# Kernel tuning notes

Hardware: AMD Instinct MI355X
Metric: run time of the kernel (lower is better)

## Reference

```python
import jax, jax.numpy as jnp
import numpy as np

EPS = 1e-12  # torch F.normalize eps

def _l2norm(x):
    n = jnp.linalg.norm(x, axis=-1, keepdims=True)
    return x / jnp.maximum(n, EPS)

def _encode(h, mask, W, b):
    # h: [B,S,H], mask: [B,S] int
    h = h * mask[..., None].astype(h.dtype)      # zero padded tokens
    pooled = h[:, 0]                             # pooling_type='cls'
    col = h[:, 1:] @ W + b                       # colbert_linear on tokens 1:
    return _l2norm(pooled), _l2norm(col)         # normalize=True


def setup_inputs() -> dict:
    key = jax.random.key(0)
    k1, k2, k3, k4, k5, k6 = jax.random.split(key, 6)
    Q, Sq, C, Sc, H, D = 64, 32, 256, 256, 768, 128
    return {
        "q_hidden": jax.random.normal(k1, (Q, Sq, H), jnp.float32),
        "c_hidden": jax.random.normal(k2, (C, Sc, H), jnp.float32),
        "W": jax.random.normal(k3, (H, D), jnp.float32) / np.sqrt(H).astype(np.float32),
        "b": jax.random.normal(k4, (D,), jnp.float32) * 0.01,
        "q_mask": jax.random.randint(k5, (Q, Sq), 0, 2, jnp.int32),
        "c_mask": jax.random.randint(k6, (C, Sc), 0, 2, jnp.int32),
    }


def reference(q_hidden, c_hidden, W, b, q_mask, c_mask):
    q_pooled, q_col = _encode(q_hidden, q_mask, W, b)   # q_col: [Q, Sq-1, D]
    c_pooled, c_col = _encode(c_hidden, c_mask, W, b)   # c_col: [C, Sc-1, D]
    # MaxSim late interaction (get_batch_colbert_sim)
    token_sim = jnp.einsum('qin,cjn->qicj', q_col, c_col)  # [Q, Sq-1, C, Sc-1]
    sim = token_sim.max(axis=-1)                           # max over doc tokens j
    denom = q_mask[:, 1:].sum(-1, keepdims=True).astype(sim.dtype)
    sim = sim.sum(axis=1) / denom                          # [Q, C]
    return sim, q_pooled, c_pooled
```

## Files before the change

### kernel.cpp

```cpp
#include <hip/hip_runtime.h>
#include <hip/hip_bf16.h>

#define QN 64
#define SQ 32
#define CN 256
#define SC 256
#define HD 768
#define DD 128

typedef __attribute__((ext_vector_type(8))) short short8;
typedef __attribute__((ext_vector_type(4))) float f32x4;

static __device__ __forceinline__ unsigned short f2bf(float x) {
  unsigned u = __float_as_uint(x);
  unsigned r = 0x7FFFu + ((u >> 16) & 1u);
  return (unsigned short)((u + r) >> 16);
}
static __device__ __forceinline__ unsigned pack2(float a, float b) {
  return (unsigned)f2bf(a) | ((unsigned)f2bf(b) << 16);
}

__global__ __launch_bounds__(256) void wcvt_kernel(const float* __restrict__ W,
                                                   unsigned short* __restrict__ Wt) {
  int d = blockIdx.x;
  for (int k = threadIdx.x; k < HD; k += 256)
    Wt[d * HD + k] = f2bf(W[(size_t)k * DD + d]);
}

__global__ __launch_bounds__(256) void pooled_kernel(
    const float* __restrict__ qh, const int* __restrict__ qm,
    const float* __restrict__ ch, const int* __restrict__ cm,
    float* __restrict__ outq, float* __restrict__ outc,
    unsigned short* __restrict__ qcolP) {
  int bid = blockIdx.x;
  const float* src;
  float* dst;
  float m;
  if (bid < QN) {
    src = qh + (size_t)bid * SQ * HD;
    m = (float)qm[bid * SQ];
    dst = outq + (size_t)bid * HD;
  } else {
    int b = bid - QN;
    src = ch + (size_t)b * SC * HD;
    m = (float)cm[b * SC];
    dst = outc + (size_t)b * HD;
  }
  int tid = threadIdx.x;
  float ss = 0.f;
  for (int k = tid; k < HD; k += 256) {
    float v = src[k] * m;
    ss += v * v;
  }
  __shared__ float red[4];
  int lane = tid & 63, wv = tid >> 6;
  for (int off = 32; off; off >>= 1) ss += __shfl_xor(ss, off);
  if (lane == 0) red[wv] = ss;
  __syncthreads();
  float tot = red[0] + red[1] + red[2] + red[3];
  float inv = 1.f / fmaxf(sqrtf(tot), 1e-12f);
  for (int k = tid; k < HD; k += 256) dst[k] = src[k] * m * inv;
  if (bid < QN && tid < 64)
    ((unsigned*)(qcolP + ((size_t)bid * 32 + 31) * DD))[tid] = 0u;
}

union ProjLDS {
  struct { unsigned short a[64 * 64]; unsigned short b[128 * 64]; } s;
  float c[64 * 132];
};

__global__ __launch_bounds__(256) void proj_kernel(
    const float* __restrict__ hidden, const int* __restrict__ mask,
    const unsigned short* __restrict__ Wt, const float* __restrict__ bias,
    unsigned short* __restrict__ out, int S, int flag) {
  __shared__ ProjLDS u;
  int tid = threadIdx.x, lane = tid & 63, w = tid >> 6;
  int lm = lane & 15, lq = lane >> 4;
  int T = S - 1;
  int wm = w & 1, wn = w >> 1;

  int ar = tid >> 2, aseg = tid & 3;
  int ag = blockIdx.x * 64 + ar;
  int ab = ag / T, at = ag - ab * T;
  const float* hrow = hidden + ((size_t)ab * S + at + 1) * HD;
  float am = (float)mask[ab * S + at + 1];
  int bd = tid >> 1, bh = tid & 1;
  const unsigned short* wrow = Wt + (size_t)bd * HD + bh * 32;

  f32x4 acc[2][4];
#pragma unroll
  for (int i = 0; i < 2; ++i)
#pragma unroll
    for (int j = 0; j < 4; ++j) acc[i][j] = (f32x4){0.f, 0.f, 0.f, 0.f};

  for (int k0 = 0; k0 < HD; k0 += 64) {
    __syncthreads();
    {
      const float4* hp = (const float4*)(hrow + k0 + aseg * 16);
      float4 v0 = hp[0], v1 = hp[1], v2 = hp[2], v3 = hp[3];
      unsigned p[8];
      p[0] = pack2(v0.x * am, v0.y * am); p[1] = pack2(v0.z * am, v0.w * am);
      p[2] = pack2(v1.x * am, v1.y * am); p[3] = pack2(v1.z * am, v1.w * am);
      p[4] = pack2(v2.x * am, v2.y * am); p[5] = pack2(v2.z * am, v2.w * am);
      p[6] = pack2(v3.x * am, v3.y * am); p[7] = pack2(v3.z * am, v3.w * am);
      int kc0 = aseg * 2;
      int pk0 = kc0 ^ (ar & 7), pk1 = (kc0 + 1) ^ (ar & 7);
      *(uint4*)&u.s.a[(ar * 8 + pk0) * 8] = *(uint4*)&p[0];
      *(uint4*)&u.s.a[(ar * 8 + pk1) * 8] = *(uint4*)&p[4];
    }
    {
      const uint4* wp = (const uint4*)(wrow + k0);
#pragma unroll
      for (int j = 0; j < 4; ++j) {
        int kc = bh * 4 + j;
        int pk = kc ^ (bd & 7);
        *(uint4*)&u.s.b[(bd * 8 + pk) * 8] = wp[j];
      }
    }
    __syncthreads();
#pragma unroll
    for (int kf = 0; kf < 2; ++kf) {
      short8 a2[2], b4[4];
#pragma unroll
      for (int mt = 0; mt < 2; ++mt) {
        int row = (wm * 2 + mt) * 16 + lm;
        int kc = kf * 4 + lq;
        a2[mt] = *(const short8*)&u.s.a[(row * 8 + (kc ^ (row & 7))) * 8];
      }
#pragma unroll
      for (int nt = 0; nt < 4; ++nt) {
        int row = (wn * 4 + nt) * 16 + lm;
        int kc = kf * 4 + lq;
        b4[nt] = *(const short8*)&u.s.b[(row * 8 + (kc ^ (row & 7))) * 8];
      }
#pragma unroll
      for (int mt = 0; mt < 2; ++mt)
#pragma unroll
        for (int nt = 0; nt < 4; ++nt)
          acc[mt][nt] = __builtin_amdgcn_mfma_f32_16x16x32_bf16(a2[mt], b4[nt], acc[mt][nt], 0, 0, 0);
    }
  }

  __syncthreads();
#pragma unroll
  for (int mt = 0; mt < 2; ++mt)
#pragma unroll
    for (int nt = 0; nt < 4; ++nt)
#pragma unroll
      for (int r = 0; r < 4; ++r) {
        int row = (wm * 2 + mt) * 16 + lq * 4 + r;
        int col = (wn * 4 + nt) * 16 + lm;
        u.c[row * 132 + col] = acc[mt][nt][r];
      }
  __syncthreads();

  int r2 = tid >> 2, seg2 = tid & 3;
  float v[32];
  float ss = 0.f;
#pragma unroll
  for (int j = 0; j < 8; ++j) {
    float4 cv = *(const float4*)&u.c[r2 * 132 + seg2 * 32 + j * 4];
    float4 bv = *(const float4*)&bias[seg2 * 32 + j * 4];
    v[4 * j + 0] = cv.x + bv.x; v[4 * j + 1] = cv.y + bv.y;
    v[4 * j + 2] = cv.z + bv.z; v[4 * j + 3] = cv.w + bv.w;
#pragma unroll
    for (int e = 0; e < 4; ++e) ss += v[4 * j + e] * v[4 * j + e];
  }
  ss += __shfl_xor(ss, 1);
  ss += __shfl_xor(ss, 2);
  float inv = 1.f / fmaxf(sqrtf(ss), 1e-12f);

  unsigned pk[16];
#pragma unroll
  for (int j = 0; j < 16; ++j) pk[j] = pack2(v[2 * j] * inv, v[2 * j + 1] * inv);

  int g = blockIdx.x * 64 + r2;
  int b = g / T, tt = g - b * T;
  unsigned short* dst;
  if (!flag)
    dst = out + ((size_t)b * 32 + tt) * DD + seg2 * 32;
  else
    dst = out + ((size_t)b * 256 + tt) * DD + seg2 * 32;
  uint4* d4 = (uint4*)dst;
  d4[0] = *(uint4*)&pk[0];  d4[1] = *(uint4*)&pk[4];
  d4[2] = *(uint4*)&pk[8];  d4[3] = *(uint4*)&pk[12];
  if (flag && tt == 254) {
    uint4* d5 = (uint4*)(dst + DD);
    d5[0] = *(uint4*)&pk[0];  d5[1] = *(uint4*)&pk[4];
    d5[2] = *(uint4*)&pk[8];  d5[3] = *(uint4*)&pk[12];
  }
}

__global__ __launch_bounds__(256, 2) void sim_kernel(
    const unsigned short* __restrict__ qcolP,
    const unsigned short* __restrict__ ccol,
    const int* __restrict__ qmask,
    float* __restrict__ sim) {
  __shared__ unsigned short cbuf[256 * 128];
  int tid = threadIdx.x, lane = tid & 63, w = tid >> 6;
  int lm = lane & 15, lq = lane >> 4;
  int q0 = blockIdx.y * 8 + w * 2;
  int c0 = blockIdx.x * 4;

  short8 af[2][2][4];
#pragma unroll
  for (int q2 = 0; q2 < 2; ++q2)
#pragma unroll
    for (int it = 0; it < 2; ++it)
#pragma unroll
      for (int kf = 0; kf < 4; ++kf)
        af[q2][it][kf] = *(const short8*)(qcolP +
            (((size_t)(q0 + q2) * 32 + it * 16 + lm) * DD + kf * 32 + lq * 8));

  float dinv[2];
#pragma unroll
  for (int q2 = 0; q2 < 2; ++q2) {
    float v = (lane >= 1 && lane < 32) ? (float)qmask[(q0 + q2) * SQ + lane] : 0.f;
    for (int off = 1; off < 64; off <<= 1) v += __shfl_xor(v, off);
    dinv[q2] = 1.f / v;
  }

  for (int cc = 0; cc < 4; ++cc) {
    int c = c0 + cc;
    __syncthreads();
    const uint4* src = (const uint4*)(ccol + (size_t)c * SC * DD);
#pragma unroll
    for (int half = 0; half < 2; ++half) {
      uint4 tmp[8];
#pragma unroll
      for (int it = 0; it < 8; ++it) tmp[it] = src[(half * 8 + it) * 256 + tid];
#pragma unroll
      for (int it = 0; it < 8; ++it) {
        int idx = (half * 8 + it) * 256 + tid;
        int row = idx >> 4, kc = idx & 15;
        int pkc = (kc & 8) | ((kc & 7) ^ (row & 7));
        *(uint4*)&cbuf[(row * 16 + pkc) * 8] = tmp[it];
      }
    }
    __syncthreads();

    float cmx[2][2][4];
#pragma unroll
    for (int q2 = 0; q2 < 2; ++q2)
#pragma unroll
      for (int it = 0; it < 2; ++it)
#pragma unroll
        for (int r = 0; r < 4; ++r) cmx[q2][it][r] = -__builtin_inff();

    for (int jt = 0; jt < 16; ++jt) {
      short8 bf[4];
#pragma unroll
      for (int kf = 0; kf < 4; ++kf) {
        int row = jt * 16 + lm;
        int kc = kf * 4 + lq;
        int pkc = (kc & 8) | ((kc & 7) ^ (row & 7));
        bf[kf] = *(const short8*)&cbuf[(row * 16 + pkc) * 8];
      }
#pragma unroll
      for (int q2 = 0; q2 < 2; ++q2)
#pragma unroll
        for (int it = 0; it < 2; ++it) {
          f32x4 acc = (f32x4){0.f, 0.f, 0.f, 0.f};
#pragma unroll
          for (int kf = 0; kf < 4; ++kf)
            acc = __builtin_amdgcn_mfma_f32_16x16x32_bf16(af[q2][it][kf], bf[kf], acc, 0, 0, 0);
#pragma unroll
          for (int r = 0; r < 4; ++r) cmx[q2][it][r] = fmaxf(cmx[q2][it][r], acc[r]);
        }
    }

#pragma unroll
    for (int q2 = 0; q2 < 2; ++q2) {
#pragma unroll
      for (int off = 1; off < 16; off <<= 1)
#pragma unroll
        for (int it = 0; it < 2; ++it)
#pragma unroll
          for (int r = 0; r < 4; ++r)
            cmx[q2][it][r] = fmaxf(cmx[q2][it][r], __shfl_xor(cmx[q2][it][r], off));
      float s = cmx[q2][0][0] + cmx[q2][0][1] + cmx[q2][0][2] + cmx[q2][0][3]
              + cmx[q2][1][0] + cmx[q2][1][1] + cmx[q2][1][2]
              + ((lq == 3) ? 0.f : cmx[q2][1][3]);
      s += __shfl_xor(s, 16);
      s += __shfl_xor(s, 32);
      if (lane == 0) sim[(q0 + q2) * CN + c] = s * dinv[q2];
    }
  }
}

extern "C" void kernel_launch(void* const* d_in, const int* in_sizes, int n_in,
                              void* d_out, int out_size, void* d_ws, size_t ws_size,
                              hipStream_t stream) {
  const float* q_hidden = (const float*)d_in[0];
  const float* c_hidden = (const float*)d_in[1];
  const float* W = (const float*)d_in[2];
  const float* bias = (const float*)d_in[3];
  const int* q_mask = (const int*)d_in[4];
  const int* c_mask = (const int*)d_in[5];

  float* out = (float*)d_out;
  float* sim = out;
  float* q_pooled = out + QN * CN;
  float* c_pooled = q_pooled + QN * HD;

  unsigned short* Wt    = (unsigned short*)d_ws;
  unsigned short* qcolP = (unsigned short*)((char*)d_ws + (256 << 10));
  unsigned short* ccol  = (unsigned short*)((char*)d_ws + (1 << 20));

  wcvt_kernel<<<DD, 256, 0, stream>>>(W, Wt);
  pooled_kernel<<<QN + CN, 256, 0, stream>>>(q_hidden, q_mask, c_hidden, c_mask,
                                             q_pooled, c_pooled, qcolP);
  proj_kernel<<<31, 256, 0, stream>>>(q_hidden, q_mask, Wt, bias, qcolP, SQ, 0);
  proj_kernel<<<1020, 256, 0, stream>>>(c_hidden, c_mask, Wt, bias, ccol, SC, 1);
  sim_kernel<<<dim3(64, 8), 256, 0, stream>>>(qcolP, ccol, q_mask, sim);
}
```

Measured before the change: 381.6 us.

## Merge prep and projection launches, prefetch proj tiles, restructure sim kernel

```diff
diff --git a/kernel.cpp b/kernel.cpp
--- a/kernel.cpp
+++ b/kernel.cpp
@@ -20,39 +20,41 @@
   return (unsigned)f2bf(a) | ((unsigned)f2bf(b) << 16);
 }
 
-__global__ __launch_bounds__(256) void wcvt_kernel(const float* __restrict__ W,
-                                                   unsigned short* __restrict__ Wt) {
-  int d = blockIdx.x;
-  for (int k = threadIdx.x; k < HD; k += 256)
-    Wt[d * HD + k] = f2bf(W[(size_t)k * DD + d]);
-}
-
-__global__ __launch_bounds__(256) void pooled_kernel(
+__global__ __launch_bounds__(256) void prep_kernel(
+    const float* __restrict__ W,
     const float* __restrict__ qh, const int* __restrict__ qm,
     const float* __restrict__ ch, const int* __restrict__ cm,
+    unsigned short* __restrict__ Wt,
     float* __restrict__ outq, float* __restrict__ outc,
     unsigned short* __restrict__ qcolP) {
-  int bid = blockIdx.x;
+  __shared__ float red[4];
+  int bid = blockIdx.x, tid = threadIdx.x;
+
+  if (bid < DD) {
+    for (int k = tid; k < HD; k += 256)
+      Wt[bid * HD + k] = f2bf(W[(size_t)k * DD + bid]);
+    return;
+  }
+
+  int row = bid - DD;
   const float* src;
   float* dst;
   float m;
-  if (bid < QN) {
-    src = qh + (size_t)bid * SQ * HD;
-    m = (float)qm[bid * SQ];
-    dst = outq + (size_t)bid * HD;
+  if (row < QN) {
+    src = qh + (size_t)row * SQ * HD;
+    m = (float)qm[row * SQ];
+    dst = outq + (size_t)row * HD;
   } else {
-    int b = bid - QN;
+    int b = row - QN;
     src = ch + (size_t)b * SC * HD;
     m = (float)cm[b * SC];
     dst = outc + (size_t)b * HD;
   }
-  int tid = threadIdx.x;
   float ss = 0.f;
   for (int k = tid; k < HD; k += 256) {
     float v = src[k] * m;
     ss += v * v;
   }
-  __shared__ float red[4];
   int lane = tid & 63, wv = tid >> 6;
   for (int off = 32; off; off >>= 1) ss += __shfl_xor(ss, off);
   if (lane == 0) red[wv] = ss;
@@ -60,8 +62,8 @@
   float tot = red[0] + red[1] + red[2] + red[3];
   float inv = 1.f / fmaxf(sqrtf(tot), 1e-12f);
   for (int k = tid; k < HD; k += 256) dst[k] = src[k] * m * inv;
-  if (bid < QN && tid < 64)
-    ((unsigned*)(qcolP + ((size_t)bid * 32 + 31) * DD))[tid] = 0u;
+  if (row < QN && tid < 64)
+    ((unsigned*)(qcolP + ((size_t)row * 32 + 31) * DD))[tid] = 0u;
 }
 
 union ProjLDS {
@@ -70,19 +72,29 @@
 };
 
 __global__ __launch_bounds__(256) void proj_kernel(
-    const float* __restrict__ hidden, const int* __restrict__ mask,
+    const float* __restrict__ q_hidden, const float* __restrict__ c_hidden,
+    const int* __restrict__ q_mask, const int* __restrict__ c_mask,
     const unsigned short* __restrict__ Wt, const float* __restrict__ bias,
-    unsigned short* __restrict__ out, int S, int flag) {
+    unsigned short* __restrict__ qcol, unsigned short* __restrict__ ccol) {
   __shared__ ProjLDS u;
+  int bx = blockIdx.x;
+  int isQ = (bx >= 1020) ? 1 : 0;
+  int base = isQ ? (bx - 1020) : bx;
+  const float* hidden = isQ ? q_hidden : c_hidden;
+  const int* mask = isQ ? q_mask : c_mask;
+  int S = isQ ? SQ : SC;
+  int T = S - 1;
+  int OUTS = isQ ? 32 : 256;
+  unsigned short* out = isQ ? qcol : ccol;
+
   int tid = threadIdx.x, lane = tid & 63, w = tid >> 6;
   int lm = lane & 15, lq = lane >> 4;
-  int T = S - 1;
   int wm = w & 1, wn = w >> 1;
 
   int ar = tid >> 2, aseg = tid & 3;
-  int ag = blockIdx.x * 64 + ar;
+  int ag = base * 64 + ar;
   int ab = ag / T, at = ag - ab * T;
-  const float* hrow = hidden + ((size_t)ab * S + at + 1) * HD;
+  const float* hrow = hidden + ((size_t)ab * S + at + 1) * HD + aseg * 16;
   float am = (float)mask[ab * S + at + 1];
   int bd = tid >> 1, bh = tid & 1;
   const unsigned short* wrow = Wt + (size_t)bd * HD + bh * 32;
@@ -93,31 +105,41 @@
 #pragma unroll
     for (int j = 0; j < 4; ++j) acc[i][j] = (f32x4){0.f, 0.f, 0.f, 0.f};
 
+  float4 va[4];
+  uint4 vb[4];
+#pragma unroll
+  for (int j = 0; j < 4; ++j) va[j] = ((const float4*)hrow)[j];
+#pragma unroll
+  for (int j = 0; j < 4; ++j) vb[j] = ((const uint4*)wrow)[j];
+
   for (int k0 = 0; k0 < HD; k0 += 64) {
     __syncthreads();
     {
-      const float4* hp = (const float4*)(hrow + k0 + aseg * 16);
-      float4 v0 = hp[0], v1 = hp[1], v2 = hp[2], v3 = hp[3];
       unsigned p[8];
-      p[0] = pack2(v0.x * am, v0.y * am); p[1] = pack2(v0.z * am, v0.w * am);
-      p[2] = pack2(v1.x * am, v1.y * am); p[3] = pack2(v1.z * am, v1.w * am);
-      p[4] = pack2(v2.x * am, v2.y * am); p[5] = pack2(v2.z * am, v2.w * am);
-      p[6] = pack2(v3.x * am, v3.y * am); p[7] = pack2(v3.z * am, v3.w * am);
+      p[0] = pack2(va[0].x * am, va[0].y * am); p[1] = pack2(va[0].z * am, va[0].w * am);
+      p[2] = pack2(va[1].x * am, va[1].y * am); p[3] = pack2(va[1].z * am, va[1].w * am);
+      p[4] = pack2(va[2].x * am, va[2].y * am); p[5] = pack2(va[2].z * am, va[2].w * am);
+      p[6] = pack2(va[3].x * am, va[3].y * am); p[7] = pack2(va[3].z * am, va[3].w * am);
       int kc0 = aseg * 2;
       int pk0 = kc0 ^ (ar & 7), pk1 = (kc0 + 1) ^ (ar & 7);
       *(uint4*)&u.s.a[(ar * 8 + pk0) * 8] = *(uint4*)&p[0];
       *(uint4*)&u.s.a[(ar * 8 + pk1) * 8] = *(uint4*)&p[4];
-    }
-    {
-      const uint4* wp = (const uint4*)(wrow + k0);
 #pragma unroll
       for (int j = 0; j < 4; ++j) {
         int kc = bh * 4 + j;
         int pk = kc ^ (bd & 7);
-        *(uint4*)&u.s.b[(bd * 8 + pk) * 8] = wp[j];
+        *(uint4*)&u.s.b[(bd * 8 + pk) * 8] = vb[j];
       }
     }
     __syncthreads();
+    if (k0 + 64 < HD) {
+      const float4* hp = (const float4*)(hrow + k0 + 64);
+      const uint4* wp = (const uint4*)(wrow + k0 + 64);
+#pragma unroll
+      for (int j = 0; j < 4; ++j) va[j] = hp[j];
+#pragma unroll
+      for (int j = 0; j < 4; ++j) vb[j] = wp[j];
+    }
 #pragma unroll
     for (int kf = 0; kf < 2; ++kf) {
       short8 a2[2], b4[4];
@@ -174,24 +196,20 @@
 #pragma unroll
   for (int j = 0; j < 16; ++j) pk[j] = pack2(v[2 * j] * inv, v[2 * j + 1] * inv);
 
-  int g = blockIdx.x * 64 + r2;
+  int g = base * 64 + r2;
   int b = g / T, tt = g - b * T;
-  unsigned short* dst;
-  if (!flag)
-    dst = out + ((size_t)b * 32 + tt) * DD + seg2 * 32;
-  else
-    dst = out + ((size_t)b * 256 + tt) * DD + seg2 * 32;
+  unsigned short* dst = out + ((size_t)b * OUTS + tt) * DD + seg2 * 32;
   uint4* d4 = (uint4*)dst;
   d4[0] = *(uint4*)&pk[0];  d4[1] = *(uint4*)&pk[4];
   d4[2] = *(uint4*)&pk[8];  d4[3] = *(uint4*)&pk[12];
-  if (flag && tt == 254) {
+  if (!isQ && tt == 254) {
     uint4* d5 = (uint4*)(dst + DD);
     d5[0] = *(uint4*)&pk[0];  d5[1] = *(uint4*)&pk[4];
     d5[2] = *(uint4*)&pk[8];  d5[3] = *(uint4*)&pk[12];
   }
 }
 
-__global__ __launch_bounds__(256, 2) void sim_kernel(
+__global__ __launch_bounds__(128, 1) void sim_kernel(
     const unsigned short* __restrict__ qcolP,
     const unsigned short* __restrict__ ccol,
     const int* __restrict__ qmask,
@@ -199,23 +217,23 @@
   __shared__ unsigned short cbuf[256 * 128];
   int tid = threadIdx.x, lane = tid & 63, w = tid >> 6;
   int lm = lane & 15, lq = lane >> 4;
-  int q0 = blockIdx.y * 8 + w * 2;
+  int qb = blockIdx.y * 8 + w * 4;
   int c0 = blockIdx.x * 4;
 
-  short8 af[2][2][4];
-#pragma unroll
-  for (int q2 = 0; q2 < 2; ++q2)
+  short8 af[4][2][4];
+#pragma unroll
+  for (int q2 = 0; q2 < 4; ++q2)
 #pragma unroll
     for (int it = 0; it < 2; ++it)
 #pragma unroll
       for (int kf = 0; kf < 4; ++kf)
         af[q2][it][kf] = *(const short8*)(qcolP +
-            (((size_t)(q0 + q2) * 32 + it * 16 + lm) * DD + kf * 32 + lq * 8));
-
-  float dinv[2];
-#pragma unroll
-  for (int q2 = 0; q2 < 2; ++q2) {
-    float v = (lane >= 1 && lane < 32) ? (float)qmask[(q0 + q2) * SQ + lane] : 0.f;
+            (((size_t)(qb + q2) * 32 + it * 16 + lm) * DD + kf * 32 + lq * 8));
+
+  float dinv[4];
+#pragma unroll
+  for (int q2 = 0; q2 < 4; ++q2) {
+    float v = (lane >= 1 && lane < 32) ? (float)qmask[(qb + q2) * SQ + lane] : 0.f;
     for (int off = 1; off < 64; off <<= 1) v += __shfl_xor(v, off);
     dinv[q2] = 1.f / v;
   }
@@ -225,13 +243,13 @@
     __syncthreads();
     const uint4* src = (const uint4*)(ccol + (size_t)c * SC * DD);
 #pragma unroll
-    for (int half = 0; half < 2; ++half) {
+    for (int g4 = 0; g4 < 4; ++g4) {
       uint4 tmp[8];
 #pragma unroll
-      for (int it = 0; it < 8; ++it) tmp[it] = src[(half * 8 + it) * 256 + tid];
+      for (int it = 0; it < 8; ++it) tmp[it] = src[(g4 * 8 + it) * 128 + tid];
 #pragma unroll
       for (int it = 0; it < 8; ++it) {
-        int idx = (half * 8 + it) * 256 + tid;
+        int idx = (g4 * 8 + it) * 128 + tid;
         int row = idx >> 4, kc = idx & 15;
         int pkc = (kc & 8) | ((kc & 7) ^ (row & 7));
         *(uint4*)&cbuf[(row * 16 + pkc) * 8] = tmp[it];
@@ -239,51 +257,41 @@
     }
     __syncthreads();
 
-    float cmx[2][2][4];
-#pragma unroll
-    for (int q2 = 0; q2 < 2; ++q2)
-#pragma unroll
-      for (int it = 0; it < 2; ++it)
-#pragma unroll
-        for (int r = 0; r < 4; ++r) cmx[q2][it][r] = -__builtin_inff();
+    float rmax[4][2];
+#pragma unroll
+    for (int q2 = 0; q2 < 4; ++q2) { rmax[q2][0] = -__builtin_inff(); rmax[q2][1] = -__builtin_inff(); }
 
     for (int jt = 0; jt < 16; ++jt) {
-      short8 bf[4];
+      short8 cf[4];
 #pragma unroll
       for (int kf = 0; kf < 4; ++kf) {
         int row = jt * 16 + lm;
         int kc = kf * 4 + lq;
         int pkc = (kc & 8) | ((kc & 7) ^ (row & 7));
-        bf[kf] = *(const short8*)&cbuf[(row * 16 + pkc) * 8];
-      }
-#pragma unroll
-      for (int q2 = 0; q2 < 2; ++q2)
+        cf[kf] = *(const short8*)&cbuf[(row * 16 + pkc) * 8];
+      }
+#pragma unroll
+      for (int q2 = 0; q2 < 4; ++q2)
 #pragma unroll
         for (int it = 0; it < 2; ++it) {
           f32x4 acc = (f32x4){0.f, 0.f, 0.f, 0.f};
 #pragma unroll
           for (int kf = 0; kf < 4; ++kf)
-            acc = __builtin_amdgcn_mfma_f32_16x16x32_bf16(af[q2][it][kf], bf[kf], acc, 0, 0, 0);
-#pragma unroll
-          for (int r = 0; r < 4; ++r) cmx[q2][it][r] = fmaxf(cmx[q2][it][r], acc[r]);
+            acc = __builtin_amdgcn_mfma_f32_16x16x32_bf16(cf[kf], af[q2][it][kf], acc, 0, 0, 0);
+          float loc = fmaxf(fmaxf(acc[0], acc[1]), fmaxf(acc[2], acc[3]));
+          rmax[q2][it] = fmaxf(rmax[q2][it], loc);
         }
     }
 
 #pragma unroll
-    for (int q2 = 0; q2 < 2; ++q2) {
-#pragma unroll
-      for (int off = 1; off < 16; off <<= 1)
-#pragma unroll
-        for (int it = 0; it < 2; ++it)
-#pragma unroll
-          for (int r = 0; r < 4; ++r)
-            cmx[q2][it][r] = fmaxf(cmx[q2][it][r], __shfl_xor(cmx[q2][it][r], off));
-      float s = cmx[q2][0][0] + cmx[q2][0][1] + cmx[q2][0][2] + cmx[q2][0][3]
-              + cmx[q2][1][0] + cmx[q2][1][1] + cmx[q2][1][2]
-              + ((lq == 3) ? 0.f : cmx[q2][1][3]);
-      s += __shfl_xor(s, 16);
-      s += __shfl_xor(s, 32);
-      if (lane == 0) sim[(q0 + q2) * CN + c] = s * dinv[q2];
+    for (int q2 = 0; q2 < 4; ++q2) {
+      float m0 = rmax[q2][0], m1 = rmax[q2][1];
+      m0 = fmaxf(m0, __shfl_xor(m0, 16)); m0 = fmaxf(m0, __shfl_xor(m0, 32));
+      m1 = fmaxf(m1, __shfl_xor(m1, 16)); m1 = fmaxf(m1, __shfl_xor(m1, 32));
+      float s = m0 + ((lm == 15) ? 0.f : m1);
+      s += __shfl_xor(s, 1); s += __shfl_xor(s, 2);
+      s += __shfl_xor(s, 4); s += __shfl_xor(s, 8);
+      if (lane == 0) sim[(qb + q2) * CN + c] = s * dinv[q2];
     }
   }
 }
@@ -307,10 +315,9 @@
   unsigned short* qcolP = (unsigned short*)((char*)d_ws + (256 << 10));
   unsigned short* ccol  = (unsigned short*)((char*)d_ws + (1 << 20));
 
-  wcvt_kernel<<<DD, 256, 0, stream>>>(W, Wt);
-  pooled_kernel<<<QN + CN, 256, 0, stream>>>(q_hidden, q_mask, c_hidden, c_mask,
-                                             q_pooled, c_pooled, qcolP);
-  proj_kernel<<<31, 256, 0, stream>>>(q_hidden, q_mask, Wt, bias, qcolP, SQ, 0);
-  proj_kernel<<<1020, 256, 0, stream>>>(c_hidden, c_mask, Wt, bias, ccol, SC, 1);
-  sim_kernel<<<dim3(64, 8), 256, 0, stream>>>(qcolP, ccol, q_mask, sim);
-}
+  prep_kernel<<<DD + QN + CN, 256, 0, stream>>>(W, q_hidden, q_mask, c_hidden, c_mask,
+                                                Wt, q_pooled, c_pooled, qcolP);
+  proj_kernel<<<1051, 256, 0, stream>>>(q_hidden, c_hidden, q_mask, c_mask,
+                                        Wt, bias, qcolP, ccol);
+  sim_kernel<<<dim3(64, 8), 128, 0, stream>>>(qcolP, ccol, q_mask, sim);
+}
```

Result: slower. 428.5 us (+12.3%).
